# Optimization experiments

Hardware: AMD Instinct MI355X
Metric: run time of the kernel (lower is better)

## Reference

```python
import jax, jax.numpy as jnp
import numpy as np

B, LQ, LK, E, H = 2, 1024, 10000, 256, 8
D = E // H  # head_dim = 32


def setup_inputs() -> dict:
    key = jax.random.key(0)
    ks = jax.random.split(key, 10)
    s = 1.0 / np.sqrt(E).astype(np.float32)
    return {
        "bev_emb": jax.random.normal(ks[0], (B, LK, E), jnp.float32),
        "queries": jax.random.normal(ks[1], (B, LQ, E), jnp.float32),
        "Wq": jax.random.normal(ks[2], (E, E), jnp.float32) * s,
        "bq": jax.random.normal(ks[3], (E,), jnp.float32) * 0.01,
        "Wk": jax.random.normal(ks[4], (E, E), jnp.float32) * s,
        "bk": jax.random.normal(ks[5], (E,), jnp.float32) * 0.01,
        "Wv": jax.random.normal(ks[6], (E, E), jnp.float32) * s,
        "bv": jax.random.normal(ks[7], (E,), jnp.float32) * 0.01,
        "Wo": jax.random.normal(ks[8], (E, E), jnp.float32) * s,
        "bo": jax.random.normal(ks[9], (E,), jnp.float32) * 0.01,
    }


def reference(bev_emb, queries, Wq, bq, Wk, bk, Wv, bv, Wo, bo):
    Bn, Lq, Em = queries.shape
    Lk = bev_emb.shape[1]
    q = (queries @ Wq + bq).reshape(Bn, Lq, H, D)
    k = (bev_emb @ Wk + bk).reshape(Bn, Lk, H, D)
    v = (bev_emb @ Wv + bv).reshape(Bn, Lk, H, D)
    # NOTE: source applies no 1/sqrt(head_dim) scaling
    energy = jnp.einsum('bqhd,bkhd->bhqk', q, k)  # [B,H,Lq,Lk]
    attn = jax.nn.softmax(energy, axis=-1)
    out = jnp.einsum('bhqk,bkhd->bqhd', attn, v).reshape(Bn, Lq, Em)
    return out @ Wo + bo
```

## Files before the change

kernel.cpp:

```cpp
#include <hip/hip_runtime.h>
#include <hip/hip_bf16.h>

#define B_  2
#define LQ_ 1024
#define LK_ 10000
#define E_  256
#define H_  8
#define D_  32
#define NT_ ((LK_ + 63) / 64)

typedef __attribute__((ext_vector_type(8))) short bf16x8;
typedef __attribute__((ext_vector_type(4))) short bf16x4;
typedef __attribute__((ext_vector_type(4))) float f32x4;

#define LOG2E 1.4426950408889634f

static __device__ __forceinline__ short bfc(float x) {
  __bf16 b = (__bf16)x;
  return __builtin_bit_cast(short, b);
}
static __device__ __forceinline__ float bf2f(short s) {
  return (float)__builtin_bit_cast(__bf16, s);
}

#if __has_builtin(__builtin_amdgcn_exp2f)
static __device__ __forceinline__ float ex2(float x) {
  return __builtin_amdgcn_exp2f(x);
}
#else
static __device__ __forceinline__ float ex2(float x) { return exp2f(x); }
#endif

#if __has_builtin(__builtin_amdgcn_mfma_f32_16x16x16bf16_1k)
static __device__ __forceinline__ f32x4 mfma_pv(bf16x4 a, bf16x4 b, f32x4 c) {
  return __builtin_amdgcn_mfma_f32_16x16x16bf16_1k(a, b, c, 0, 0, 0);
}
#else
static __device__ __forceinline__ f32x4 mfma_pv(bf16x4 a, bf16x4 b, f32x4 c) {
  asm volatile("s_nop 1\n\tv_mfma_f32_16x16x16_bf16 %0, %1, %2, %0"
               : "+v"(c) : "v"(a), "v"(b));
  return c;
}
#endif

static __device__ __forceinline__ int xcd_swizzle(int flat, int nwg) {
  const int xcd = flat & 7, rest = flat >> 3;
  const int q = nwg >> 3, r = nwg & 7;
  return (xcd < r ? xcd * (q + 1) : r * (q + 1) + (xcd - r) * q) + rest;
}

static __device__ __forceinline__ void split8(const float4& a, const float4& b,
                                              bf16x8& hi, bf16x8& lo) {
  float v[8] = {a.x, a.y, a.z, a.w, b.x, b.y, b.z, b.w};
#pragma unroll
  for (int i = 0; i < 8; ++i) {
    const short h = bfc(v[i]);
    hi[i] = h;
    lo[i] = bfc(v[i] - bf2f(h));
  }
}

__global__ __launch_bounds__(256) void wtrans4(
    const float* __restrict__ W0, const float* __restrict__ W1,
    const float* __restrict__ W2, const float* __restrict__ W3,
    unsigned short* __restrict__ T0, unsigned short* __restrict__ T1,
    unsigned short* __restrict__ T2, unsigned short* __restrict__ T3) {
  const float* W;
  unsigned short* T;
  switch (blockIdx.z) {
    case 0:  W = W0; T = T0; break;
    case 1:  W = W1; T = T1; break;
    case 2:  W = W2; T = T2; break;
    default: W = W3; T = T3; break;
  }
  __shared__ float ts[16][17];
  const int tx = threadIdx.x & 15;
  const int ty = threadIdx.x >> 4;
  const int k0 = blockIdx.x * 16;
  const int n0 = blockIdx.y * 16;
  ts[ty][tx] = W[(size_t)(k0 + ty) * 256 + n0 + tx];
  __syncthreads();
  T[(size_t)(n0 + ty) * 256 + k0 + tx] = (unsigned short)bfc(ts[tx][ty]);
}

template <bool KV, bool F32OUT>
__global__ __launch_bounds__(256) void proj_wave(
    const float* __restrict__ A,
    const unsigned short* __restrict__ Wt1,
    const unsigned short* __restrict__ Wt2,
    const float* __restrict__ b1, const float* __restrict__ b2,
    void* __restrict__ C1v, void* __restrict__ C2v) {
  const int lane = threadIdx.x & 63;
  const int nt   = threadIdx.x >> 6;
  const int mt   = blockIdx.x;
  const int lr   = lane & 15;
  const int oc   = lane >> 4;
  const int m0   = mt * 32;
  const int n0   = nt * 64;

  f32x4 ac1[2][4];
  f32x4 ac2[2][4];
#pragma unroll
  for (int s = 0; s < 2; ++s)
#pragma unroll
    for (int q = 0; q < 4; ++q) {
      ac1[s][q] = (f32x4){0.f, 0.f, 0.f, 0.f};
      if (KV) ac2[s][q] = (f32x4){0.f, 0.f, 0.f, 0.f};
    }

  const float* a0p = &A[(size_t)(m0 + lr) * 256 + oc * 8];
  const float* a1p = a0p + 16 * 256;

  float4 c0a = *(const float4*)(a0p + 0);
  float4 c0b = *(const float4*)(a0p + 4);
  float4 c1a = *(const float4*)(a1p + 0);
  float4 c1b = *(const float4*)(a1p + 4);

  for (int kb = 0; kb < 8; ++kb) {
    bf16x8 ah0, al0, ah1, al1;
    split8(c0a, c0b, ah0, al0);
    split8(c1a, c1b, ah1, al1);

    const size_t wko = (size_t)(kb * 32 + oc * 8);
    bf16x8 w1[4], w2[4];
#pragma unroll
    for (int q = 0; q < 4; ++q) {
      w1[q] = *(const bf16x8*)&Wt1[(size_t)(n0 + q * 16 + lr) * 256 + wko];
      if (KV) w2[q] = *(const bf16x8*)&Wt2[(size_t)(n0 + q * 16 + lr) * 256 + wko];
    }

    if (kb < 7) {
      c0a = *(const float4*)(a0p + (kb + 1) * 32 + 0);
      c0b = *(const float4*)(a0p + (kb + 1) * 32 + 4);
      c1a = *(const float4*)(a1p + (kb + 1) * 32 + 0);
      c1b = *(const float4*)(a1p + (kb + 1) * 32 + 4);
    }

#pragma unroll
    for (int q = 0; q < 4; ++q) {
      ac1[0][q] = __builtin_amdgcn_mfma_f32_16x16x32_bf16(w1[q], ah0, ac1[0][q], 0, 0, 0);
      ac1[0][q] = __builtin_amdgcn_mfma_f32_16x16x32_bf16(w1[q], al0, ac1[0][q], 0, 0, 0);
      ac1[1][q] = __builtin_amdgcn_mfma_f32_16x16x32_bf16(w1[q], ah1, ac1[1][q], 0, 0, 0);
      ac1[1][q] = __builtin_amdgcn_mfma_f32_16x16x32_bf16(w1[q], al1, ac1[1][q], 0, 0, 0);
      if (KV) {
        ac2[0][q] = __builtin_amdgcn_mfma_f32_16x16x32_bf16(w2[q], ah0, ac2[0][q], 0, 0, 0);
        ac2[1][q] = __builtin_amdgcn_mfma_f32_16x16x32_bf16(w2[q], ah1, ac2[1][q], 0, 0, 0);
      }
    }
  }

#pragma unroll
  for (int s = 0; s < 2; ++s) {
#pragma unroll
    for (int q = 0; q < 4; ++q) {
      const int m = m0 + s * 16 + lr;
      const int n = n0 + q * 16 + oc * 4;
      const float4 bv1 = *(const float4*)&b1[n];
      if (F32OUT) {
        float4 o;
        o.x = ac1[s][q][0] + bv1.x; o.y = ac1[s][q][1] + bv1.y;
        o.z = ac1[s][q][2] + bv1.z; o.w = ac1[s][q][3] + bv1.w;
        *(float4*)&((float*)C1v)[(size_t)m * 256 + n] = o;
      } else {
        ushort4 o;
        o.x = (unsigned short)bfc(ac1[s][q][0] + bv1.x);
        o.y = (unsigned short)bfc(ac1[s][q][1] + bv1.y);
        o.z = (unsigned short)bfc(ac1[s][q][2] + bv1.z);
        o.w = (unsigned short)bfc(ac1[s][q][3] + bv1.w);
        *(ushort4*)&((unsigned short*)C1v)[(size_t)m * 256 + n] = o;
      }
      if (KV) {
        const float4 bv2 = *(const float4*)&b2[n];
        ushort4 o;
        o.x = (unsigned short)bfc(ac2[s][q][0] + bv2.x);
        o.y = (unsigned short)bfc(ac2[s][q][1] + bv2.y);
        o.z = (unsigned short)bfc(ac2[s][q][2] + bv2.z);
        o.w = (unsigned short)bfc(ac2[s][q][3] + bv2.w);
        *(ushort4*)&((unsigned short*)C2v)[(size_t)m * 256 + n] = o;
      }
    }
  }
}

__global__ __launch_bounds__(256) void attn_mfma(const float* __restrict__ q,
                                                 const unsigned short* __restrict__ kbf,
                                                 const unsigned short* __restrict__ vbf,
                                                 float* __restrict__ Opart,
                                                 float* __restrict__ lpart,
                                                 float* __restrict__ o_direct,
                                                 int tiles_per_split, int nsplit) {
  const int nwg = 64 * gridDim.z;
  const int l   = xcd_swizzle(blockIdx.x + 8 * (blockIdx.y + 8 * blockIdx.z), nwg);
  const int qb   = l & 7;
  const int h    = (l >> 3) & 7;
  const int z    = l >> 6;
  const int s_id = z / B_;
  const int b    = z % B_;
  const int t    = threadIdx.x;
  const int lane = t & 63;
  const int w    = t >> 6;
  const int lq   = lane & 15;
  const int grp  = lane >> 4;

  __shared__ ushort Klds[2][64][64];
  __shared__ ushort Vtld[2][32][64];

  const int t0 = s_id * tiles_per_split;
  const int t1 = min(NT_, t0 + tiles_per_split);

  const int qrowA = qb * 128 + w * 32 + lq;
  const int qrowB = qrowA + 16;
  bf16x8 qfA, qfB;
  {
    const float* qpA = &q[((size_t)(b * LQ_ + qrowA)) * E_ + h * D_ + grp * 8];
    const float* qpB = &q[((size_t)(b * LQ_ + qrowB)) * E_ + h * D_ + grp * 8];
    const float4 a0 = *(const float4*)qpA;
    const float4 a1 = *(const float4*)(qpA + 4);
    const float4 b0 = *(const float4*)qpB;
    const float4 b1 = *(const float4*)(qpB + 4);
    qfA[0] = bfc(a0.x * LOG2E); qfA[1] = bfc(a0.y * LOG2E);
    qfA[2] = bfc(a0.z * LOG2E); qfA[3] = bfc(a0.w * LOG2E);
    qfA[4] = bfc(a1.x * LOG2E); qfA[5] = bfc(a1.y * LOG2E);
    qfA[6] = bfc(a1.z * LOG2E); qfA[7] = bfc(a1.w * LOG2E);
    qfB[0] = bfc(b0.x * LOG2E); qfB[1] = bfc(b0.y * LOG2E);
    qfB[2] = bfc(b0.z * LOG2E); qfB[3] = bfc(b0.w * LOG2E);
    qfB[4] = bfc(b1.x * LOG2E); qfB[5] = bfc(b1.y * LOG2E);
    qfB[6] = bfc(b1.z * LOG2E); qfB[7] = bfc(b1.w * LOG2E);
  }

  const int krow_l = t >> 2;
  const int kchunk = t & 3;
  const int vkp    = t >> 3;
  const int vd     = (t & 7) * 4;

  float lA = 0.f, lB = 0.f;
  f32x4 a0A = {0.f, 0.f, 0.f, 0.f}, a1A = {0.f, 0.f, 0.f, 0.f};
  f32x4 a0B = {0.f, 0.f, 0.f, 0.f}, a1B = {0.f, 0.f, 0.f, 0.f};

  const size_t kvrow0 = (size_t)b * LK_;

  uint4 kval; ushort4 v0, v1;
  auto load_tile = [&](int kn) {
    if (kn == NT_ - 1) {
      const int krow  = min(kn * 64 + krow_l, LK_ - 1);
      const int vrow0 = min(kn * 64 + 2 * vkp, LK_ - 1);
      const int vrow1 = min(kn * 64 + 2 * vkp + 1, LK_ - 1);
      kval = *(const uint4*)&kbf[(kvrow0 + krow) * E_ + h * D_ + kchunk * 8];
      v0 = *(const ushort4*)&vbf[(kvrow0 + vrow0) * E_ + h * D_ + vd];
      v1 = *(const ushort4*)&vbf[(kvrow0 + vrow1) * E_ + h * D_ + vd];
    } else {
      kval = *(const uint4*)&kbf[(kvrow0 + kn * 64 + krow_l) * E_ + h * D_ + kchunk * 8];
      v0 = *(const ushort4*)&vbf[(kvrow0 + kn * 64 + 2 * vkp) * E_ + h * D_ + vd];
      v1 = *(const ushort4*)&vbf[(kvrow0 + kn * 64 + 2 * vkp + 1) * E_ + h * D_ + vd];
    }
  };
  auto store_tile = [&](int buf) {
    *(uint4*)((char*)&Klds[buf][krow_l][0] + ((kchunk * 16) ^ ((krow_l & 7) << 4))) = kval;
#pragma unroll
    for (int i = 0; i < 4; ++i) {
      const int d = vd + i;
      *(ushort2*)((char*)&Vtld[buf][d][0] + ((vkp * 4) ^ ((d & 7) << 4))) =
          make_ushort2(((const unsigned short*)&v0)[i], ((const unsigned short*)&v1)[i]);
    }
  };

  load_tile(t0);
  store_tile(0);
  if (t0 + 1 < t1) load_tile(t0 + 1);
  __syncthreads();

  int cur = 0;
  for (int kt = t0; kt < t1; ++kt) {
    const int rem = LK_ - kt * 64;

    if (kt + 1 < t1) store_tile(cur ^ 1);
    if (kt + 2 < t1) load_tile(kt + 2);

    f32x4 pA[4], pB[4];
    __builtin_amdgcn_s_setprio(1);
#pragma unroll
    for (int s = 0; s < 4; ++s) {
      const int row = s * 16 + lq;
      const bf16x8 kf = *(const bf16x8*)((const char*)&Klds[cur][row][0] +
                                         ((grp * 16) ^ ((row & 7) << 4)));
      const f32x4 zero = {0.f, 0.f, 0.f, 0.f};
      pA[s] = __builtin_amdgcn_mfma_f32_16x16x32_bf16(kf, qfA, zero, 0, 0, 0);
      pB[s] = __builtin_amdgcn_mfma_f32_16x16x32_bf16(kf, qfB, zero, 0, 0, 0);
    }
    __builtin_amdgcn_s_setprio(0);

    bf16x4 pbA[4], pbB[4];
    if (rem >= 64) {
#pragma unroll
      for (int s = 0; s < 4; ++s)
#pragma unroll
        for (int r = 0; r < 4; ++r) {
          const float eA = ex2(pA[s][r]);
          const float eB = ex2(pB[s][r]);
          lA += eA; lB += eB;
          pbA[s][r] = bfc(eA); pbB[s][r] = bfc(eB);
        }
    } else {
#pragma unroll
      for (int s = 0; s < 4; ++s) {
        const bool vs = (s * 16 + grp * 4) < rem;
#pragma unroll
        for (int r = 0; r < 4; ++r) {
          const float eA = vs ? ex2(pA[s][r]) : 0.f;
          const float eB = vs ? ex2(pB[s][r]) : 0.f;
          lA += eA; lB += eB;
          pbA[s][r] = bfc(eA); pbB[s][r] = bfc(eB);
        }
      }
    }

    __builtin_amdgcn_s_setprio(1);
#pragma unroll
    for (int s = 0; s < 4; ++s) {
      {
        const int row = lq;
        const bf16x4 vf = *(const bf16x4*)((const char*)&Vtld[cur][row][0] +
                                           ((s * 32 + grp * 8) ^ ((row & 7) << 4)));
        a0A = mfma_pv(vf, pbA[s], a0A);
        a0B = mfma_pv(vf, pbB[s], a0B);
      }
      {
        const int row = 16 + lq;
        const bf16x4 vf = *(const bf16x4*)((const char*)&Vtld[cur][row][0] +
                                           ((s * 32 + grp * 8) ^ ((row & 7) << 4)));
        a1A = mfma_pv(vf, pbA[s], a1A);
        a1B = mfma_pv(vf, pbB[s], a1B);
      }
    }
    __builtin_amdgcn_s_setprio(0);

    __syncthreads();
    cur ^= 1;
  }

  lA += __shfl_xor(lA, 16);
  lA += __shfl_xor(lA, 32);
  lB += __shfl_xor(lB, 16);
  lB += __shfl_xor(lB, 32);

  if (nsplit == 1) {
    const float invA = 1.f / lA;
    const float invB = 1.f / lB;
    float* opA = &o_direct[((size_t)(b * LQ_ + qrowA)) * E_ + h * D_];
    float* opB = &o_direct[((size_t)(b * LQ_ + qrowB)) * E_ + h * D_];
#pragma unroll
    for (int r = 0; r < 4; ++r) {
      opA[grp * 4 + r]      = a0A[r] * invA;
      opA[16 + grp * 4 + r] = a1A[r] * invA;
      opB[grp * 4 + r]      = a0B[r] * invB;
      opB[16 + grp * 4 + r] = a1B[r] * invB;
    }
  } else {
    const size_t pbA =
        (size_t)s_id * (B_ * H_ * LQ_) + ((size_t)b * H_ + h) * LQ_ + qrowA;
    const size_t pbB = pbA + 16;
#pragma unroll
    for (int r = 0; r < 4; ++r) {
      Opart[pbA * D_ + grp * 4 + r]      = a0A[r];
      Opart[pbA * D_ + 16 + grp * 4 + r] = a1A[r];
      Opart[pbB * D_ + grp * 4 + r]      = a0B[r];
      Opart[pbB * D_ + 16 + grp * 4 + r] = a1B[r];
    }
    if (grp == 0) {
      lpart[pbA] = lA;
      lpart[pbB] = lB;
    }
  }
}

__global__ __launch_bounds__(256) void attn_merge(const float* __restrict__ Opart,
                                                  const float* __restrict__ lpart,
                                                  float* __restrict__ o, int S) {
  const int idx = blockIdx.x * 256 + threadIdx.x;
  if (idx >= B_ * LQ_ * E_) return;
  const int e   = idx & (E_ - 1);
  const int row = idx >> 8;
  const int b   = row >> 10;
  const int qq  = row & (LQ_ - 1);
  const int h   = e >> 5;
  const int d   = e & (D_ - 1);
  const size_t base   = ((size_t)b * H_ + h) * LQ_ + qq;
  const size_t stride = (size_t)B_ * H_ * LQ_;

  float lsum = 0.f, osum = 0.f;
  for (int s = 0; s < S; ++s) {
    lsum += lpart[s * stride + base];
    osum += Opart[(s * stride + base) * D_ + d];
  }
  o[idx] = osum / lsum;
}

extern "C" void kernel_launch(void* const* d_in, const int* in_sizes, int n_in,
                              void* d_out, int out_size, void* d_ws, size_t ws_size,
                              hipStream_t stream) {
  const float* bev     = (const float*)d_in[0];
  const float* queries = (const float*)d_in[1];
  const float* Wq      = (const float*)d_in[2];
  const float* bq      = (const float*)d_in[3];
  const float* Wk      = (const float*)d_in[4];
  const float* bk      = (const float*)d_in[5];
  const float* Wv      = (const float*)d_in[6];
  const float* bv      = (const float*)d_in[7];
  const float* Wo      = (const float*)d_in[8];
  const float* bo      = (const float*)d_in[9];
  float* out = (float*)d_out;

  const size_t nq = (size_t)B_ * LQ_ * E_;
  const size_t nk = (size_t)B_ * LK_ * E_;
  const size_t nw = (size_t)E_ * E_;
  float*          qws = (float*)d_ws;
  unsigned short* kbf = (unsigned short*)(qws + nq);
  unsigned short* vbf = kbf + nk;
  float*          ows = (float*)(vbf + nk);
  unsigned short* Wtq = (unsigned short*)(ows + nq);
  unsigned short* Wtk = Wtq + nw;
  unsigned short* Wtv = Wtk + nw;
  unsigned short* Wto = Wtv + nw;
  float*          opart = (float*)(Wto + nw);

  const size_t base_bytes = (nq * 2) * sizeof(float) +
                            (nk * 2 + nw * 4) * sizeof(unsigned short);
  const size_t per_split_bytes = (size_t)B_ * H_ * LQ_ * (D_ + 1) * sizeof(float);
  int S = 0;
  for (int cand = 8; cand >= 1; cand >>= 1) {
    if (base_bytes + (size_t)cand * per_split_bytes <= ws_size) { S = cand; break; }
  }

  wtrans4<<<dim3(16, 16, 4), 256, 0, stream>>>(Wq, Wk, Wv, Wo, Wtq, Wtk, Wtv, Wto);

  proj_wave<false, true><<<dim3(64), 256, 0, stream>>>(
      queries, Wtq, nullptr, bq, nullptr, qws, nullptr);
  proj_wave<true, false><<<dim3(625), 256, 0, stream>>>(
      bev, Wtk, Wtv, bk, bv, kbf, vbf);

  if (S <= 1) {
    attn_mfma<<<dim3(8, H_, B_), 256, 0, stream>>>(
        qws, kbf, vbf, nullptr, nullptr, ows, NT_, 1);
  } else {
    float* lpart = opart + (size_t)S * B_ * H_ * LQ_ * D_;
    const int tps = (NT_ + S - 1) / S;
    attn_mfma<<<dim3(8, H_, B_ * S), 256, 0, stream>>>(
        qws, kbf, vbf, opart, lpart, nullptr, tps, S);
    attn_merge<<<dim3((B_ * LQ_ * E_ + 255) / 256), 256, 0, stream>>>(
        opart, lpart, ows, S);
  }

  proj_wave<false, true><<<dim3(64), 256, 0, stream>>>(
      ows, Wto, nullptr, bo, nullptr, out, nullptr);
}
```

Baseline: 128.4 us.

## Compute softmax row sums via MFMA with ones and interleave PV per slice

Replaces the per-lane scalar accumulation of exponentials and the final cross-lane shuffles with an extra MFMA that multiplies the bf16 probabilities by a vector of ones, so row sums come out of the matrix unit. It also fuses the exp/convert step with the PV MFMAs per 16-key slice, which drops the per-tile probability arrays and the separate PV loop with its priority bumps. Launch bounds now request 4 blocks per CU to cap register use. Sums are now taken over bf16-rounded probabilities, which matches the PV numerator but changes rounding, and the extra MFMAs add matrix-unit work.

```diff
diff --git a/kernel.cpp b/kernel.cpp
--- a/kernel.cpp
+++ b/kernel.cpp
@@ -182,13 +182,13 @@
   }
 }
 
-__global__ __launch_bounds__(256) void attn_mfma(const float* __restrict__ q,
-                                                 const unsigned short* __restrict__ kbf,
-                                                 const unsigned short* __restrict__ vbf,
-                                                 float* __restrict__ Opart,
-                                                 float* __restrict__ lpart,
-                                                 float* __restrict__ o_direct,
-                                                 int tiles_per_split, int nsplit) {
+__global__ __launch_bounds__(256, 4) void attn_mfma(const float* __restrict__ q,
+                                                    const unsigned short* __restrict__ kbf,
+                                                    const unsigned short* __restrict__ vbf,
+                                                    float* __restrict__ Opart,
+                                                    float* __restrict__ lpart,
+                                                    float* __restrict__ o_direct,
+                                                    int tiles_per_split, int nsplit) {
   const int nwg = 64 * gridDim.z;
   const int l   = xcd_swizzle(blockIdx.x + 8 * (blockIdx.y + 8 * blockIdx.z), nwg);
   const int qb   = l & 7;
@@ -233,9 +233,10 @@
   const int vkp    = t >> 3;
   const int vd     = (t & 7) * 4;
 
-  float lA = 0.f, lB = 0.f;
   f32x4 a0A = {0.f, 0.f, 0.f, 0.f}, a1A = {0.f, 0.f, 0.f, 0.f};
   f32x4 a0B = {0.f, 0.f, 0.f, 0.f}, a1B = {0.f, 0.f, 0.f, 0.f};
+  f32x4 accLA = {0.f, 0.f, 0.f, 0.f}, accLB = {0.f, 0.f, 0.f, 0.f};
+  const bf16x4 ones = {(short)0x3F80, (short)0x3F80, (short)0x3F80, (short)0x3F80};
 
   const size_t kvrow0 = (size_t)b * LK_;
 
@@ -289,59 +290,67 @@
     }
     __builtin_amdgcn_s_setprio(0);
 
-    bf16x4 pbA[4], pbB[4];
     if (rem >= 64) {
 #pragma unroll
-      for (int s = 0; s < 4; ++s)
+      for (int s = 0; s < 4; ++s) {
+        bf16x4 pbA, pbB;
 #pragma unroll
         for (int r = 0; r < 4; ++r) {
-          const float eA = ex2(pA[s][r]);
-          const float eB = ex2(pB[s][r]);
-          lA += eA; lB += eB;
-          pbA[s][r] = bfc(eA); pbB[s][r] = bfc(eB);
-        }
+          pbA[r] = bfc(ex2(pA[s][r]));
+          pbB[r] = bfc(ex2(pB[s][r]));
+        }
+        accLA = mfma_pv(ones, pbA, accLA);
+        accLB = mfma_pv(ones, pbB, accLB);
+        {
+          const int row = lq;
+          const bf16x4 vf = *(const bf16x4*)((const char*)&Vtld[cur][row][0] +
+                                             ((s * 32 + grp * 8) ^ ((row & 7) << 4)));
+          a0A = mfma_pv(vf, pbA, a0A);
+          a0B = mfma_pv(vf, pbB, a0B);
+        }
+        {
+          const int row = 16 + lq;
+          const bf16x4 vf = *(const bf16x4*)((const char*)&Vtld[cur][row][0] +
+                                             ((s * 32 + grp * 8) ^ ((row & 7) << 4)));
+          a1A = mfma_pv(vf, pbA, a1A);
+          a1B = mfma_pv(vf, pbB, a1B);
+        }
+      }
     } else {
 #pragma unroll
       for (int s = 0; s < 4; ++s) {
         const bool vs = (s * 16 + grp * 4) < rem;
+        bf16x4 pbA, pbB;
 #pragma unroll
         for (int r = 0; r < 4; ++r) {
-          const float eA = vs ? ex2(pA[s][r]) : 0.f;
-          const float eB = vs ? ex2(pB[s][r]) : 0.f;
-          lA += eA; lB += eB;
-          pbA[s][r] = bfc(eA); pbB[s][r] = bfc(eB);
+          pbA[r] = vs ? bfc(ex2(pA[s][r])) : (short)0;
+          pbB[r] = vs ? bfc(ex2(pB[s][r])) : (short)0;
+        }
+        accLA = mfma_pv(ones, pbA, accLA);
+        accLB = mfma_pv(ones, pbB, accLB);
+        {
+          const int row = lq;
+          const bf16x4 vf = *(const bf16x4*)((const char*)&Vtld[cur][row][0] +
+                                             ((s * 32 + grp * 8) ^ ((row & 7) << 4)));
+          a0A = mfma_pv(vf, pbA, a0A);
+          a0B = mfma_pv(vf, pbB, a0B);
+        }
+        {
+          const int row = 16 + lq;
+          const bf16x4 vf = *(const bf16x4*)((const char*)&Vtld[cur][row][0] +
+                                             ((s * 32 + grp * 8) ^ ((row & 7) << 4)));
+          a1A = mfma_pv(vf, pbA, a1A);
+          a1B = mfma_pv(vf, pbB, a1B);
         }
       }
     }
-
-    __builtin_amdgcn_s_setprio(1);
-#pragma unroll
-    for (int s = 0; s < 4; ++s) {
-      {
-        const int row = lq;
-        const bf16x4 vf = *(const bf16x4*)((const char*)&Vtld[cur][row][0] +
-                                           ((s * 32 + grp * 8) ^ ((row & 7) << 4)));
-        a0A = mfma_pv(vf, pbA[s], a0A);
-        a0B = mfma_pv(vf, pbB[s], a0B);
-      }
-      {
-        const int row = 16 + lq;
-        const bf16x4 vf = *(const bf16x4*)((const char*)&Vtld[cur][row][0] +
-                                           ((s * 32 + grp * 8) ^ ((row & 7) << 4)));
-        a1A = mfma_pv(vf, pbA[s], a1A);
-        a1B = mfma_pv(vf, pbB[s], a1B);
-      }
-    }
-    __builtin_amdgcn_s_setprio(0);
 
     __syncthreads();
     cur ^= 1;
   }
 
-  lA += __shfl_xor(lA, 16);
-  lA += __shfl_xor(lA, 32);
-  lB += __shfl_xor(lB, 16);
-  lB += __shfl_xor(lB, 32);
+  const float lA = accLA[0];
+  const float lB = accLB[0];
 
   if (nsplit == 1) {
     const float invA = 1.f / lA;
```

After: 134.6 us. 1.05x slower.
